# Kernel tuning notes

Measured on AMD Instinct MI355X. Metric: run time of the kernel, lower is better.

Reference implementation:

```python
import jax, jax.numpy as jnp
import numpy as np

N = 50000   # nodes
E = 800000  # edges (avg degree 16)
D0 = 256    # input feat dim
H1, D1 = 4, 64  # layer1 heads, per-head dim
H2, D2 = 4, 64  # layer2 heads, per-head dim
NEG_SLOPE = 0.2


def setup_inputs() -> dict:
    key = jax.random.key(0)
    ks = jax.random.split(key, 9)
    s = 0.1
    feature = jax.random.normal(ks[0], (N, D0), jnp.float32)
    src = jax.random.randint(ks[1], (E,), 0, N, dtype=jnp.int32)
    dst = jax.random.randint(ks[2], (E,), 0, N, dtype=jnp.int32)
    W1 = jax.random.normal(ks[3], (D0, H1 * D1), jnp.float32) * s
    al1 = jax.random.normal(ks[4], (H1, D1), jnp.float32) * s
    ar1 = jax.random.normal(ks[5], (H1, D1), jnp.float32) * s
    W2 = jax.random.normal(ks[6], (H1 * D1, H2 * D2), jnp.float32) * s
    al2 = jax.random.normal(ks[7], (H2, D2), jnp.float32) * s
    ar2 = jax.random.normal(ks[8], (H2, D2), jnp.float32) * s
    return dict(feature=feature, W1=W1, al1=al1, ar1=ar1,
                W2=W2, al2=al2, ar2=ar2, src=src, dst=dst)


def gat_conv(x, W, al, ar, src, dst, H, d, act):
    # x: [N, in]; W: [in, H*d]; al, ar: [H, d]
    feat = (x @ W).reshape(N, H, d)                 # [N,H,d]
    el = jnp.einsum('nhd,hd->nh', feat, al)         # [N,H] src-side score
    er = jnp.einsum('nhd,hd->nh', feat, ar)         # [N,H] dst-side score
    e = jax.nn.leaky_relu(el[src] + er[dst], NEG_SLOPE)  # [E,H]
    # segment softmax over edges grouped by destination node
    m = jax.ops.segment_max(e, dst, num_segments=N)      # [N,H]
    ex = jnp.exp(e - m[dst])                             # [E,H]
    denom = jax.ops.segment_sum(ex, dst, num_segments=N) # [N,H]
    alpha = ex / jnp.maximum(denom[dst], 1e-9)           # [E,H]
    msg = feat[src] * alpha[..., None]                   # [E,H,d]
    out = jax.ops.segment_sum(msg, dst, num_segments=N)  # [N,H,d]
    return act(out)


def reference(feature, W1, al1, ar1, W2, al2, ar2, src, dst):
    h = gat_conv(feature, W1, al1, ar1, src, dst, H1, D1, jax.nn.elu)  # [N,H1,D1]
    h = h.reshape(N, H1 * D1)                                          # concat heads
    h = gat_conv(h, W2, al2, ar2, src, dst, H2, D2, lambda x: x)       # [N,H2,D2]
    return h.mean(axis=1)                                              # mean over heads -> [N,D2]
```

## Files before the change

### kernel.cpp

```cpp
#include <hip/hip_runtime.h>
#include <hip/hip_fp16.h>
#include <math.h>
#include <stdint.h>

#define NNODES 50000
#define NEDGES 800000
#define DIM 256
#define HEADS 4
#define DH 64
#define NEG_SLOPE 0.2f

typedef _Float16 half8 __attribute__((ext_vector_type(8)));
typedef float floatx4 __attribute__((ext_vector_type(4)));

static __device__ __forceinline__ float h2f(unsigned short h) {
  __half x = *(const __half*)&h;
  return __half2float(x);
}
static __device__ __forceinline__ unsigned short f2h(float f) {
  __half x = __float2half(f);
  return *(const unsigned short*)&x;
}

__global__ __launch_bounds__(256) void wt_k(const float* __restrict__ W,
                                            _Float16* __restrict__ WT) {
  int n = blockIdx.x;
  int k = threadIdx.x;
  WT[n * 256 + k] = (_Float16)W[k * 256 + n];
}

template <typename AT>
__global__ __launch_bounds__(256) void gemm_k(const AT* __restrict__ A,
                                              const _Float16* __restrict__ BT,
                                              const float* __restrict__ alw,
                                              const float* __restrict__ arw,
                                              unsigned short* __restrict__ Cb,
                                              float* __restrict__ el,
                                              float* __restrict__ er, int M) {
  __shared__ __attribute__((aligned(16))) _Float16 Asl[64][32];
  __shared__ __attribute__((aligned(16))) _Float16 Bsl[256][32];
  int t = threadIdx.x;
  int lane = t & 63, w = t >> 6;
  int m16 = lane & 15, q = lane >> 4;
  int row0 = blockIdx.x * 64;
  floatx4 acc[4][4];
#pragma unroll
  for (int i = 0; i < 4; ++i)
#pragma unroll
    for (int j = 0; j < 4; ++j) acc[i][j] = (floatx4){0.f, 0.f, 0.f, 0.f};

  float alv[4], arv[4];
#pragma unroll
  for (int ni = 0; ni < 4; ++ni) {
    alv[ni] = alw[w * 64 + ni * 16 + m16];
    arv[ni] = arw[w * 64 + ni * 16 + m16];
  }

  int arow = t >> 2, akoff = (t & 3) * 8;

  for (int k0 = 0; k0 < DIM; k0 += 32) {
    if constexpr (sizeof(AT) == 4) {
      float4 x0 = make_float4(0.f, 0.f, 0.f, 0.f);
      float4 x1 = make_float4(0.f, 0.f, 0.f, 0.f);
      if (row0 + arow < M) {
        const float* ap = (const float*)&A[(size_t)(row0 + arow) * DIM + k0 + akoff];
        x0 = *(const float4*)ap;
        x1 = *(const float4*)(ap + 4);
      }
      _Float16* as = &Asl[arow][akoff];
      as[0] = (_Float16)x0.x; as[1] = (_Float16)x0.y;
      as[2] = (_Float16)x0.z; as[3] = (_Float16)x0.w;
      as[4] = (_Float16)x1.x; as[5] = (_Float16)x1.y;
      as[6] = (_Float16)x1.z; as[7] = (_Float16)x1.w;
    } else {
      int4 x = make_int4(0, 0, 0, 0);
      if (row0 + arow < M)
        x = *(const int4*)&A[(size_t)(row0 + arow) * DIM + k0 + akoff];
      *(int4*)&Asl[arow][akoff] = x;
    }
    {
      const _Float16* bp = &BT[(size_t)t * 256 + k0];
      *(int4*)&Bsl[t][0] = *(const int4*)bp;
      *(int4*)&Bsl[t][8] = *(const int4*)(bp + 8);
      *(int4*)&Bsl[t][16] = *(const int4*)(bp + 16);
      *(int4*)&Bsl[t][24] = *(const int4*)(bp + 24);
    }
    __syncthreads();
    half8 af[4], bf[4];
#pragma unroll
    for (int i = 0; i < 4; ++i) af[i] = *(const half8*)&Asl[i * 16 + m16][q * 8];
#pragma unroll
    for (int i = 0; i < 4; ++i)
      bf[i] = *(const half8*)&Bsl[w * 64 + i * 16 + m16][q * 8];
#pragma unroll
    for (int mi = 0; mi < 4; ++mi)
#pragma unroll
      for (int ni = 0; ni < 4; ++ni)
        acc[mi][ni] = __builtin_amdgcn_mfma_f32_16x16x32_f16(
            af[mi], bf[ni], acc[mi][ni], 0, 0, 0);
    __syncthreads();
  }
#pragma unroll
  for (int mi = 0; mi < 4; ++mi) {
#pragma unroll
    for (int r = 0; r < 4; ++r) {
      float pl = acc[mi][0][r] * alv[0] + acc[mi][1][r] * alv[1] +
                 acc[mi][2][r] * alv[2] + acc[mi][3][r] * alv[3];
      float pr = acc[mi][0][r] * arv[0] + acc[mi][1][r] * arv[1] +
                 acc[mi][2][r] * arv[2] + acc[mi][3][r] * arv[3];
#pragma unroll
      for (int off = 1; off < 16; off <<= 1) {
        pl += __shfl_xor(pl, off, 64);
        pr += __shfl_xor(pr, off, 64);
      }
      int row = row0 + mi * 16 + q * 4 + r;
      if (m16 == 0 && row < M) {
        el[row * HEADS + w] = pl;
        er[row * HEADS + w] = pr;
      }
    }
  }
#pragma unroll
  for (int mi = 0; mi < 4; ++mi) {
#pragma unroll
    for (int r = 0; r < 4; ++r) {
      int row = row0 + mi * 16 + q * 4 + r;
      if (row < M) {
#pragma unroll
        for (int ni = 0; ni < 4; ++ni)
          Cb[(size_t)row * DIM + w * 64 + ni * 16 + m16] = f2h(acc[mi][ni][r]);
      }
    }
  }
}

__global__ __launch_bounds__(256) void deg_k(const int* __restrict__ dst,
                                             int* __restrict__ deg) {
  int e = blockIdx.x * 256 + threadIdx.x;
  if (e < NEDGES) atomicAdd(&deg[dst[e]], 1);
}

__global__ __launch_bounds__(1024) void scan_k(const int* __restrict__ deg,
                                               int* __restrict__ row_ptr,
                                               int* __restrict__ cursor, int n) {
  __shared__ int wsum[16];
  __shared__ int wpref[16];
  int t = threadIdx.x, lane = t & 63, w = t >> 6;
  int running = 0;
  for (int base = 0; base < n; base += 4096) {
    int idx0 = base + t * 4;
    int4 v = make_int4(0, 0, 0, 0);
    if (idx0 + 3 < n) v = *(const int4*)&deg[idx0];
    else {
      if (idx0 < n) v.x = deg[idx0];
      if (idx0 + 1 < n) v.y = deg[idx0 + 1];
      if (idx0 + 2 < n) v.z = deg[idx0 + 2];
    }
    int s0 = v.x, s1 = s0 + v.y, s2 = s1 + v.z, s3 = s2 + v.w;
    int incl = s3;
#pragma unroll
    for (int off = 1; off < 64; off <<= 1) {
      int u = __shfl_up(incl, off, 64);
      if (lane >= off) incl += u;
    }
    if (lane == 63) wsum[w] = incl;
    __syncthreads();
    if (w == 0 && lane < 16) {
      int x = wsum[lane];
#pragma unroll
      for (int off = 1; off < 16; off <<= 1) {
        int u = __shfl_up(x, off, 64);
        if (lane >= off) x += u;
      }
      wpref[lane] = x;
    }
    __syncthreads();
    int wbase = (w == 0) ? 0 : wpref[w - 1];
    int texcl = incl - s3 + wbase + running;
    if (idx0 < n)     { row_ptr[idx0]     = texcl;      cursor[idx0]     = texcl; }
    if (idx0 + 1 < n) { row_ptr[idx0 + 1] = texcl + s0; cursor[idx0 + 1] = texcl + s0; }
    if (idx0 + 2 < n) { row_ptr[idx0 + 2] = texcl + s1; cursor[idx0 + 2] = texcl + s1; }
    if (idx0 + 3 < n) { row_ptr[idx0 + 3] = texcl + s2; cursor[idx0 + 3] = texcl + s2; }
    int tot = wpref[15];
    __syncthreads();
    running += tot;
  }
  if (t == 0) row_ptr[n] = running;
}

__global__ __launch_bounds__(256) void scatter_k(const int* __restrict__ src,
                                                 const int* __restrict__ dst,
                                                 int* __restrict__ cursor,
                                                 int* __restrict__ srcoff) {
  int e = blockIdx.x * 256 + threadIdx.x;
  if (e < NEDGES) {
    int pos = atomicAdd(&cursor[dst[e]], 1);
    srcoff[pos] = src[e] << 9;
  }
}

template <int MODE>
__global__ __launch_bounds__(256) void agg_k(const unsigned short* __restrict__ feat,
                                             const float* __restrict__ el,
                                             const float* __restrict__ er,
                                             const int* __restrict__ row_ptr,
                                             const int* __restrict__ srcoff,
                                             void* __restrict__ outp) {
  int lane = threadIdx.x & 63;
  int w = threadIdx.x >> 6;
  int n = blockIdx.x * 4 + w;
  if (n >= NNODES) return;
  int h = lane >> 4;
  int hsel = lane & 3;
  int esel = lane >> 2;
  int beg = row_ptr[n], end = row_ptr[n + 1];
  float erv = er[n * HEADS + hsel];
  int laneByte = lane * 8;
  const char* fb = (const char*)feat;
  const char* elb = (const char*)el;
  float a0 = 0.f, a1 = 0.f, a2 = 0.f, a3 = 0.f, sume = 0.f;
  for (int c0 = beg; c0 < end; c0 += 16) {
    int soff = 0;
    if (lane < 16 && c0 + lane < end) soff = srcoff[c0 + lane];
    float av = 0.f;
    if (c0 + esel < end) {
      int sE = __shfl(soff, esel, 64);
      float elv = *(const float*)(elb + (sE >> 5) + hsel * 4);
      float v = elv + erv;
      v = v > 0.f ? v : NEG_SLOPE * v;
      av = __expf(v);
    }
    for (int j4 = 0; j4 < 16; j4 += 4) {
      if (c0 + j4 >= end) break;
#pragma unroll
      for (int jj = 0; jj < 4; ++jj) {
        int j = j4 + jj;
        int sB = __shfl(soff, j, 64);
        float a = __shfl(av, 4 * j + h, 64);
        ushort4 u = *(const ushort4*)(fb + (sB + laneByte));
        a0 += h2f(u.x) * a;
        a1 += h2f(u.y) * a;
        a2 += h2f(u.z) * a;
        a3 += h2f(u.w) * a;
        sume += a;
      }
    }
  }
  float inv = 1.f / fmaxf(sume, 1e-9f);
  a0 *= inv; a1 *= inv; a2 *= inv; a3 *= inv;
  if (MODE == 1) {
    a0 = a0 > 0.f ? a0 : (__expf(a0) - 1.f);
    a1 = a1 > 0.f ? a1 : (__expf(a1) - 1.f);
    a2 = a2 > 0.f ? a2 : (__expf(a2) - 1.f);
    a3 = a3 > 0.f ? a3 : (__expf(a3) - 1.f);
    ushort4 o;
    o.x = f2h(a0); o.y = f2h(a1); o.z = f2h(a2); o.w = f2h(a3);
    *(ushort4*)((char*)outp + (size_t)n * 512 + laneByte) = o;
  } else {
    a0 += __shfl_xor(a0, 16, 64); a0 += __shfl_xor(a0, 32, 64);
    a1 += __shfl_xor(a1, 16, 64); a1 += __shfl_xor(a1, 32, 64);
    a2 += __shfl_xor(a2, 16, 64); a2 += __shfl_xor(a2, 32, 64);
    a3 += __shfl_xor(a3, 16, 64); a3 += __shfl_xor(a3, 32, 64);
    if (lane < 16) {
      float4 o = make_float4(a0 * 0.25f, a1 * 0.25f, a2 * 0.25f, a3 * 0.25f);
      *(float4*)((float*)outp + (size_t)n * 64 + lane * 4) = o;
    }
  }
}

extern "C" void kernel_launch(void* const* d_in, const int* in_sizes, int n_in,
                              void* d_out, int out_size, void* d_ws, size_t ws_size,
                              hipStream_t stream) {
  const float* feature = (const float*)d_in[0];
  const float* W1 = (const float*)d_in[1];
  const float* al1 = (const float*)d_in[2];
  const float* ar1 = (const float*)d_in[3];
  const float* W2 = (const float*)d_in[4];
  const float* al2 = (const float*)d_in[5];
  const float* ar2 = (const float*)d_in[6];
  const int* src = (const int*)d_in[7];
  const int* dst = (const int*)d_in[8];
  float* out = (float*)d_out;

  uintptr_t p = (uintptr_t)d_ws;
  auto alloc = [&](size_t bytes) -> void* {
    uintptr_t cur = (p + 255) & ~(uintptr_t)255;
    p = cur + bytes;
    return (void*)cur;
  };
  unsigned short* featH = (unsigned short*)alloc((size_t)NNODES * DIM * 2);
  unsigned short* hidH  = (unsigned short*)alloc((size_t)NNODES * DIM * 2);
  _Float16* WT1 = (_Float16*)alloc((size_t)256 * 256 * 2);
  _Float16* WT2 = (_Float16*)alloc((size_t)256 * 256 * 2);
  float* el    = (float*)alloc((size_t)NNODES * HEADS * 4);
  float* er    = (float*)alloc((size_t)NNODES * HEADS * 4);
  int* deg     = (int*)alloc((size_t)NNODES * 4);
  int* row_ptr = (int*)alloc((size_t)(NNODES + 1) * 4);
  int* cursor  = (int*)alloc((size_t)NNODES * 4);
  int* srcoff  = (int*)alloc((size_t)NEDGES * 4);

  const int EB = (NEDGES + 255) / 256;
  const int MB = (NNODES + 63) / 64;
  const int AB = (NNODES + 3) / 4;

  wt_k<<<256, 256, 0, stream>>>(W1, WT1);
  wt_k<<<256, 256, 0, stream>>>(W2, WT2);
  hipMemsetAsync(deg, 0, (size_t)NNODES * 4, stream);
  deg_k<<<EB, 256, 0, stream>>>(dst, deg);
  scan_k<<<1, 1024, 0, stream>>>(deg, row_ptr, cursor, NNODES);
  scatter_k<<<EB, 256, 0, stream>>>(src, dst, cursor, srcoff);

  gemm_k<float><<<MB, 256, 0, stream>>>(feature, WT1, al1, ar1, featH, el, er, NNODES);
  agg_k<1><<<AB, 256, 0, stream>>>(featH, el, er, row_ptr, srcoff, hidH);

  gemm_k<_Float16><<<MB, 256, 0, stream>>>((const _Float16*)hidH, WT2, al2, ar2,
                                           featH, el, er, NNODES);
  agg_k<2><<<AB, 256, 0, stream>>>(featH, el, er, row_ptr, srcoff, out);
}
```

Before: 404.9 us.

## Parallelize CSR scan, pad sentinels in aggregation, swap GEMM operands, vectorize edge kernels

Replaces the single-block degree scan with a three-kernel multi-block scan. Pads srcoff, el and featH with a sentinel node so the aggregation loop runs full 16-edge chunks with no bounds checks. Each lane now computes its own attention weight per edge instead of shuffling precomputed ones. The GEMM swaps MFMA operand order so the epilogue writes ushort4 rows, pads LDS rows to avoid bank conflicts, and merges the two weight-transpose launches. Edge kernels also load four edges at once. The cost is redundant exp computation per lane and extra sentinel loads on partial chunks.

```diff
diff --git a/kernel.cpp b/kernel.cpp
--- a/kernel.cpp
+++ b/kernel.cpp
@@ -10,6 +10,9 @@
 #define DH 64
 #define NEG_SLOPE 0.2f
 
+#define CSR_NPB 1024
+#define CSR_NB ((NNODES + CSR_NPB - 1) / CSR_NPB)
+
 typedef _Float16 half8 __attribute__((ext_vector_type(8)));
 typedef float floatx4 __attribute__((ext_vector_type(4)));
 
@@ -22,9 +25,14 @@
   return *(const unsigned short*)&x;
 }
 
-__global__ __launch_bounds__(256) void wt_k(const float* __restrict__ W,
-                                            _Float16* __restrict__ WT) {
-  int n = blockIdx.x;
+__global__ __launch_bounds__(256) void wt_k(const float* __restrict__ W1,
+                                            const float* __restrict__ W2,
+                                            _Float16* __restrict__ WT1,
+                                            _Float16* __restrict__ WT2) {
+  int b = blockIdx.x;
+  const float* W = (b < 256) ? W1 : W2;
+  _Float16* WT = (b < 256) ? WT1 : WT2;
+  int n = b & 255;
   int k = threadIdx.x;
   WT[n * 256 + k] = (_Float16)W[k * 256 + n];
 }
@@ -37,8 +45,8 @@
                                               unsigned short* __restrict__ Cb,
                                               float* __restrict__ el,
                                               float* __restrict__ er, int M) {
-  __shared__ __attribute__((aligned(16))) _Float16 Asl[64][32];
-  __shared__ __attribute__((aligned(16))) _Float16 Bsl[256][32];
+  __shared__ __attribute__((aligned(16))) _Float16 Asl[64][40];
+  __shared__ __attribute__((aligned(16))) _Float16 Bsl[256][40];
   int t = threadIdx.x;
   int lane = t & 63, w = t >> 6;
   int m16 = lane & 15, q = lane >> 4;
@@ -49,11 +57,11 @@
 #pragma unroll
     for (int j = 0; j < 4; ++j) acc[i][j] = (floatx4){0.f, 0.f, 0.f, 0.f};
 
-  float alv[4], arv[4];
+  float4 alv[4], arv[4];
 #pragma unroll
   for (int ni = 0; ni < 4; ++ni) {
-    alv[ni] = alw[w * 64 + ni * 16 + m16];
-    arv[ni] = arw[w * 64 + ni * 16 + m16];
+    alv[ni] = *(const float4*)&alw[w * 64 + ni * 16 + q * 4];
+    arv[ni] = *(const float4*)&arw[w * 64 + ni * 16 + q * 4];
   }
 
   int arow = t >> 2, akoff = (t & 3) * 8;
@@ -67,11 +75,12 @@
         x0 = *(const float4*)ap;
         x1 = *(const float4*)(ap + 4);
       }
-      _Float16* as = &Asl[arow][akoff];
-      as[0] = (_Float16)x0.x; as[1] = (_Float16)x0.y;
-      as[2] = (_Float16)x0.z; as[3] = (_Float16)x0.w;
-      as[4] = (_Float16)x1.x; as[5] = (_Float16)x1.y;
-      as[6] = (_Float16)x1.z; as[7] = (_Float16)x1.w;
+      half8 hv;
+      hv[0] = (_Float16)x0.x; hv[1] = (_Float16)x0.y;
+      hv[2] = (_Float16)x0.z; hv[3] = (_Float16)x0.w;
+      hv[4] = (_Float16)x1.x; hv[5] = (_Float16)x1.y;
+      hv[6] = (_Float16)x1.z; hv[7] = (_Float16)x1.w;
+      *(half8*)&Asl[arow][akoff] = hv;
     } else {
       int4 x = make_int4(0, 0, 0, 0);
       if (row0 + arow < M)
@@ -86,49 +95,44 @@
       *(int4*)&Bsl[t][24] = *(const int4*)(bp + 24);
     }
     __syncthreads();
-    half8 af[4], bf[4];
+    half8 wf[4], af[4];
+#pragma unroll
+    for (int i = 0; i < 4; ++i)
+      wf[i] = *(const half8*)&Bsl[w * 64 + i * 16 + m16][q * 8];
 #pragma unroll
     for (int i = 0; i < 4; ++i) af[i] = *(const half8*)&Asl[i * 16 + m16][q * 8];
-#pragma unroll
-    for (int i = 0; i < 4; ++i)
-      bf[i] = *(const half8*)&Bsl[w * 64 + i * 16 + m16][q * 8];
 #pragma unroll
     for (int mi = 0; mi < 4; ++mi)
 #pragma unroll
       for (int ni = 0; ni < 4; ++ni)
         acc[mi][ni] = __builtin_amdgcn_mfma_f32_16x16x32_f16(
-            af[mi], bf[ni], acc[mi][ni], 0, 0, 0);
+            wf[ni], af[mi], acc[mi][ni], 0, 0, 0);
     __syncthreads();
   }
 #pragma unroll
   for (int mi = 0; mi < 4; ++mi) {
-#pragma unroll
-    for (int r = 0; r < 4; ++r) {
-      float pl = acc[mi][0][r] * alv[0] + acc[mi][1][r] * alv[1] +
-                 acc[mi][2][r] * alv[2] + acc[mi][3][r] * alv[3];
-      float pr = acc[mi][0][r] * arv[0] + acc[mi][1][r] * arv[1] +
-                 acc[mi][2][r] * arv[2] + acc[mi][3][r] * arv[3];
-#pragma unroll
-      for (int off = 1; off < 16; off <<= 1) {
-        pl += __shfl_xor(pl, off, 64);
-        pr += __shfl_xor(pr, off, 64);
-      }
-      int row = row0 + mi * 16 + q * 4 + r;
-      if (m16 == 0 && row < M) {
-        el[row * HEADS + w] = pl;
-        er[row * HEADS + w] = pr;
-      }
-    }
-  }
-#pragma unroll
-  for (int mi = 0; mi < 4; ++mi) {
-#pragma unroll
-    for (int r = 0; r < 4; ++r) {
-      int row = row0 + mi * 16 + q * 4 + r;
-      if (row < M) {
-#pragma unroll
-        for (int ni = 0; ni < 4; ++ni)
-          Cb[(size_t)row * DIM + w * 64 + ni * 16 + m16] = f2h(acc[mi][ni][r]);
+    int node = row0 + mi * 16 + m16;
+    float pl = 0.f, pr = 0.f;
+#pragma unroll
+    for (int ni = 0; ni < 4; ++ni) {
+      pl += acc[mi][ni][0] * alv[ni].x + acc[mi][ni][1] * alv[ni].y +
+            acc[mi][ni][2] * alv[ni].z + acc[mi][ni][3] * alv[ni].w;
+      pr += acc[mi][ni][0] * arv[ni].x + acc[mi][ni][1] * arv[ni].y +
+            acc[mi][ni][2] * arv[ni].z + acc[mi][ni][3] * arv[ni].w;
+    }
+    pl += __shfl_xor(pl, 16, 64); pl += __shfl_xor(pl, 32, 64);
+    pr += __shfl_xor(pr, 16, 64); pr += __shfl_xor(pr, 32, 64);
+    if (q == 0 && node < M) {
+      el[node * HEADS + w] = pl;
+      er[node * HEADS + w] = pr;
+    }
+    if (node < M) {
+#pragma unroll
+      for (int ni = 0; ni < 4; ++ni) {
+        ushort4 o;
+        o.x = f2h(acc[mi][ni][0]); o.y = f2h(acc[mi][ni][1]);
+        o.z = f2h(acc[mi][ni][2]); o.w = f2h(acc[mi][ni][3]);
+        *(ushort4*)&Cb[(size_t)node * DIM + w * 64 + ni * 16 + q * 4] = o;
       }
     }
   }
@@ -136,66 +140,95 @@
 
 __global__ __launch_bounds__(256) void deg_k(const int* __restrict__ dst,
                                              int* __restrict__ deg) {
-  int e = blockIdx.x * 256 + threadIdx.x;
-  if (e < NEDGES) atomicAdd(&deg[dst[e]], 1);
-}
-
-__global__ __launch_bounds__(1024) void scan_k(const int* __restrict__ deg,
-                                               int* __restrict__ row_ptr,
-                                               int* __restrict__ cursor, int n) {
-  __shared__ int wsum[16];
-  __shared__ int wpref[16];
+  int e4 = (blockIdx.x * 256 + threadIdx.x) * 4;
+  if (e4 < NEDGES) {
+    int4 d = *(const int4*)&dst[e4];
+    atomicAdd(&deg[d.x], 1);
+    atomicAdd(&deg[d.y], 1);
+    atomicAdd(&deg[d.z], 1);
+    atomicAdd(&deg[d.w], 1);
+  }
+}
+
+__global__ __launch_bounds__(256) void csr_part_k(const int* __restrict__ deg,
+                                                  int* __restrict__ bsum) {
+  __shared__ int ws[4];
   int t = threadIdx.x, lane = t & 63, w = t >> 6;
-  int running = 0;
-  for (int base = 0; base < n; base += 4096) {
-    int idx0 = base + t * 4;
-    int4 v = make_int4(0, 0, 0, 0);
-    if (idx0 + 3 < n) v = *(const int4*)&deg[idx0];
-    else {
-      if (idx0 < n) v.x = deg[idx0];
-      if (idx0 + 1 < n) v.y = deg[idx0 + 1];
-      if (idx0 + 2 < n) v.z = deg[idx0 + 2];
-    }
-    int s0 = v.x, s1 = s0 + v.y, s2 = s1 + v.z, s3 = s2 + v.w;
-    int incl = s3;
-#pragma unroll
-    for (int off = 1; off < 64; off <<= 1) {
-      int u = __shfl_up(incl, off, 64);
-      if (lane >= off) incl += u;
-    }
-    if (lane == 63) wsum[w] = incl;
-    __syncthreads();
-    if (w == 0 && lane < 16) {
-      int x = wsum[lane];
-#pragma unroll
-      for (int off = 1; off < 16; off <<= 1) {
-        int u = __shfl_up(x, off, 64);
-        if (lane >= off) x += u;
-      }
-      wpref[lane] = x;
-    }
-    __syncthreads();
-    int wbase = (w == 0) ? 0 : wpref[w - 1];
-    int texcl = incl - s3 + wbase + running;
-    if (idx0 < n)     { row_ptr[idx0]     = texcl;      cursor[idx0]     = texcl; }
-    if (idx0 + 1 < n) { row_ptr[idx0 + 1] = texcl + s0; cursor[idx0 + 1] = texcl + s0; }
-    if (idx0 + 2 < n) { row_ptr[idx0 + 2] = texcl + s1; cursor[idx0 + 2] = texcl + s1; }
-    if (idx0 + 3 < n) { row_ptr[idx0 + 3] = texcl + s2; cursor[idx0 + 3] = texcl + s2; }
-    int tot = wpref[15];
-    __syncthreads();
-    running += tot;
-  }
-  if (t == 0) row_ptr[n] = running;
+  int idx = blockIdx.x * CSR_NPB + t * 4;
+  int s = 0;
+  if (idx < NNODES) {
+    int4 v = *(const int4*)&deg[idx];
+    s = v.x + v.y + v.z + v.w;
+  }
+#pragma unroll
+  for (int off = 1; off < 64; off <<= 1) s += __shfl_xor(s, off, 64);
+  if (lane == 0) ws[w] = s;
+  __syncthreads();
+  if (t == 0) bsum[blockIdx.x] = ws[0] + ws[1] + ws[2] + ws[3];
+}
+
+__global__ __launch_bounds__(64) void csr_mid_k(const int* __restrict__ bsum,
+                                                int* __restrict__ bbase,
+                                                int* __restrict__ row_ptr,
+                                                float* __restrict__ el,
+                                                int* __restrict__ srcoff) {
+  int t = threadIdx.x;
+  int v = (t < CSR_NB) ? bsum[t] : 0;
+  int incl = v;
+#pragma unroll
+  for (int off = 1; off < 64; off <<= 1) {
+    int u = __shfl_up(incl, off, 64);
+    if (t >= off) incl += u;
+  }
+  if (t < CSR_NB) bbase[t] = incl - v;
+  if (t == 0) row_ptr[NNODES] = NEDGES;
+  if (t < HEADS) el[NNODES * HEADS + t] = -1e30f;
+  if (t < 16) srcoff[NEDGES + t] = NNODES << 9;
+}
+
+__global__ __launch_bounds__(256) void csr_emit_k(const int* __restrict__ deg,
+                                                  const int* __restrict__ bbase,
+                                                  int* __restrict__ row_ptr,
+                                                  int* __restrict__ cursor) {
+  __shared__ int ws[4];
+  int t = threadIdx.x, lane = t & 63, w = t >> 6;
+  int idx = blockIdx.x * CSR_NPB + t * 4;
+  int4 v = make_int4(0, 0, 0, 0);
+  if (idx < NNODES) v = *(const int4*)&deg[idx];
+  int s0 = v.x, s1 = s0 + v.y, s2 = s1 + v.z, s3 = s2 + v.w;
+  int incl = s3;
+#pragma unroll
+  for (int off = 1; off < 64; off <<= 1) {
+    int u = __shfl_up(incl, off, 64);
+    if (lane >= off) incl += u;
+  }
+  if (lane == 63) ws[w] = incl;
+  __syncthreads();
+  int wbase = 0;
+#pragma unroll
+  for (int i = 0; i < 4; ++i)
+    if (i < w) wbase += ws[i];
+  int base = bbase[blockIdx.x] + wbase + incl - s3;
+  if (idx < NNODES) {
+    int4 rp = make_int4(base, base + s0, base + s1, base + s2);
+    *(int4*)&row_ptr[idx] = rp;
+    *(int4*)&cursor[idx] = rp;
+  }
 }
 
 __global__ __launch_bounds__(256) void scatter_k(const int* __restrict__ src,
                                                  const int* __restrict__ dst,
                                                  int* __restrict__ cursor,
                                                  int* __restrict__ srcoff) {
-  int e = blockIdx.x * 256 + threadIdx.x;
-  if (e < NEDGES) {
-    int pos = atomicAdd(&cursor[dst[e]], 1);
-    srcoff[pos] = src[e] << 9;
+  int e4 = (blockIdx.x * 256 + threadIdx.x) * 4;
+  if (e4 < NEDGES) {
+    int4 s = *(const int4*)&src[e4];
+    int4 d = *(const int4*)&dst[e4];
+    int p;
+    p = atomicAdd(&cursor[d.x], 1); srcoff[p] = s.x << 9;
+    p = atomicAdd(&cursor[d.y], 1); srcoff[p] = s.y << 9;
+    p = atomicAdd(&cursor[d.z], 1); srcoff[p] = s.z << 9;
+    p = atomicAdd(&cursor[d.w], 1); srcoff[p] = s.w << 9;
   }
 }
 
@@ -209,41 +242,32 @@
   int lane = threadIdx.x & 63;
   int w = threadIdx.x >> 6;
   int n = blockIdx.x * 4 + w;
-  if (n >= NNODES) return;
   int h = lane >> 4;
-  int hsel = lane & 3;
-  int esel = lane >> 2;
-  int beg = row_ptr[n], end = row_ptr[n + 1];
-  float erv = er[n * HEADS + hsel];
+  int beg = __builtin_amdgcn_readfirstlane(row_ptr[n]);
+  int end = __builtin_amdgcn_readfirstlane(row_ptr[n + 1]);
+  float erv = er[n * HEADS + h];
   int laneByte = lane * 8;
+  int h4 = h * 4;
   const char* fb = (const char*)feat;
   const char* elb = (const char*)el;
   float a0 = 0.f, a1 = 0.f, a2 = 0.f, a3 = 0.f, sume = 0.f;
   for (int c0 = beg; c0 < end; c0 += 16) {
-    int soff = 0;
-    if (lane < 16 && c0 + lane < end) soff = srcoff[c0 + lane];
-    float av = 0.f;
-    if (c0 + esel < end) {
-      int sE = __shfl(soff, esel, 64);
-      float elv = *(const float*)(elb + (sE >> 5) + hsel * 4);
-      float v = elv + erv;
-      v = v > 0.f ? v : NEG_SLOPE * v;
-      av = __expf(v);
-    }
-    for (int j4 = 0; j4 < 16; j4 += 4) {
-      if (c0 + j4 >= end) break;
-#pragma unroll
-      for (int jj = 0; jj < 4; ++jj) {
-        int j = j4 + jj;
-        int sB = __shfl(soff, j, 64);
-        float a = __shfl(av, 4 * j + h, 64);
-        ushort4 u = *(const ushort4*)(fb + (sB + laneByte));
-        a0 += h2f(u.x) * a;
-        a1 += h2f(u.y) * a;
-        a2 += h2f(u.z) * a;
-        a3 += h2f(u.w) * a;
-        sume += a;
-      }
+    int idx = c0 + (lane & 15);
+    if (idx >= end) idx = NEDGES;
+    int sv = srcoff[idx];
+#pragma unroll
+    for (int j = 0; j < 16; ++j) {
+      int sj = __builtin_amdgcn_readlane(sv, j);
+      float elv = *(const float*)(elb + (sj >> 5) + h4);
+      float vv = elv + erv;
+      vv = fmaxf(vv, NEG_SLOPE * vv);
+      float a = __expf(vv);
+      ushort4 u = *(const ushort4*)(fb + sj + laneByte);
+      a0 += h2f(u.x) * a;
+      a1 += h2f(u.y) * a;
+      a2 += h2f(u.z) * a;
+      a3 += h2f(u.w) * a;
+      sume += a;
     }
   }
   float inv = 1.f / fmaxf(sume, 1e-9f);
@@ -288,27 +312,30 @@
     p = cur + bytes;
     return (void*)cur;
   };
-  unsigned short* featH = (unsigned short*)alloc((size_t)NNODES * DIM * 2);
+  unsigned short* featH = (unsigned short*)alloc((size_t)(NNODES + 1) * DIM * 2);
   unsigned short* hidH  = (unsigned short*)alloc((size_t)NNODES * DIM * 2);
   _Float16* WT1 = (_Float16*)alloc((size_t)256 * 256 * 2);
   _Float16* WT2 = (_Float16*)alloc((size_t)256 * 256 * 2);
-  float* el    = (float*)alloc((size_t)NNODES * HEADS * 4);
+  float* el    = (float*)alloc((size_t)(NNODES + 1) * HEADS * 4);
   float* er    = (float*)alloc((size_t)NNODES * HEADS * 4);
   int* deg     = (int*)alloc((size_t)NNODES * 4);
   int* row_ptr = (int*)alloc((size_t)(NNODES + 1) * 4);
   int* cursor  = (int*)alloc((size_t)NNODES * 4);
-  int* srcoff  = (int*)alloc((size_t)NEDGES * 4);
-
-  const int EB = (NEDGES + 255) / 256;
+  int* srcoff  = (int*)alloc((size_t)(NEDGES + 16) * 4);
+  int* bsum    = (int*)alloc((size_t)CSR_NB * 4);
+  int* bbase   = (int*)alloc((size_t)CSR_NB * 4);
+
+  const int E4B = (NEDGES / 4 + 255) / 256;
   const int MB = (NNODES + 63) / 64;
-  const int AB = (NNODES + 3) / 4;
-
-  wt_k<<<256, 256, 0, stream>>>(W1, WT1);
-  wt_k<<<256, 256, 0, stream>>>(W2, WT2);
+  const int AB = NNODES / 4;
+
+  wt_k<<<512, 256, 0, stream>>>(W1, W2, WT1, WT2);
   hipMemsetAsync(deg, 0, (size_t)NNODES * 4, stream);
-  deg_k<<<EB, 256, 0, stream>>>(dst, deg);
-  scan_k<<<1, 1024, 0, stream>>>(deg, row_ptr, cursor, NNODES);
-  scatter_k<<<EB, 256, 0, stream>>>(src, dst, cursor, srcoff);
+  deg_k<<<E4B, 256, 0, stream>>>(dst, deg);
+  csr_part_k<<<CSR_NB, 256, 0, stream>>>(deg, bsum);
+  csr_mid_k<<<1, 64, 0, stream>>>(bsum, bbase, row_ptr, el, srcoff);
+  csr_emit_k<<<CSR_NB, 256, 0, stream>>>(deg, bbase, row_ptr, cursor);
+  scatter_k<<<E4B, 256, 0, stream>>>(src, dst, cursor, srcoff);
 
   gemm_k<float><<<MB, 256, 0, stream>>>(feature, WT1, al1, ar1, featH, el, er, NNODES);
   agg_k<1><<<AB, 256, 0, stream>>>(featH, el, er, row_ptr, srcoff, hidH);
```

After: 470.0 us. +16.1%, slower.
